# Kernel tuning notes

Hardware: AMD Instinct MI355X
Metric: run time of the kernel (lower is better)

Reference implementation:

```python
import jax, jax.numpy as jnp
import numpy as np

NUM_WIRES = 20
DEPTH = 4


def setup_inputs() -> dict:
    key = jax.random.key(0)
    x = jax.random.normal(key, (NUM_WIRES,), dtype=jnp.float32)
    return {"x": x}


def _apply_1q(state, gate, wire):
    # state: flat [2^n] complex; apply 2x2 gate on `wire`
    s = state.reshape(2 ** wire, 2, -1)
    return jnp.einsum('ab,ibj->iaj', gate, s).reshape(-1)


def _apply_cnot(state, control):
    # CNOT on adjacent wires (control, control+1): flip target where control==1
    s = state.reshape(2 ** control, 2, 2, -1)
    s = jnp.concatenate([s[:, :1], s[:, 1:, ::-1]], axis=1)
    return s.reshape(-1)


def _simulate(x):
    n = NUM_WIRES
    state = jnp.zeros(2 ** n, dtype=jnp.complex64).at[0].set(1.0)
    half = (x.astype(jnp.float32) * 0.5)
    c = jnp.cos(half).astype(jnp.complex64)  # [n]
    s = jnp.sin(half).astype(jnp.complex64)  # [n]
    for _ in range(DEPTH):
        for w in range(n):
            cw, sw = c[w], s[w]
            rx = jnp.stack([jnp.stack([cw, -1j * sw]), jnp.stack([-1j * sw, cw])])
            ry = jnp.stack([jnp.stack([cw, -sw]), jnp.stack([sw, cw])])
            state = _apply_1q(state, rx, w)
            state = _apply_1q(state, ry, w)
        for w in range(n - 1):
            state = _apply_cnot(state, w)
    probs = jnp.abs(state) ** 2  # real float32 [2^n]
    expz = []
    for i in range(n):
        p = probs.reshape(2 ** i, 2, -1).sum(axis=(0, 2))
        expz.append(p[0] - p[1])
    return jnp.stack(expz).astype(jnp.float32)  # [n] <Z_i>


def reference(x):
    return _simulate(x)
```

## Files before the change

kernel.cpp:

```cpp
#include <hip/hip_runtime.h>


#define NW 20

__device__ __forceinline__ float2 cmul(float2 a, float2 b) {
    return make_float2(a.x*b.x - a.y*b.y, a.x*b.y + a.y*b.x);
}

__device__ __forceinline__ void apply_gate(float2& a0, float2& a1,
                                           float2 u00, float2 u01,
                                           float2 u10, float2 u11) {
    float2 b0, b1;
    b0.x = u00.x*a0.x - u00.y*a0.y + u01.x*a1.x - u01.y*a1.y;
    b0.y = u00.x*a0.y + u00.y*a0.x + u01.x*a1.y + u01.y*a1.x;
    b1.x = u10.x*a0.x - u10.y*a0.y + u11.x*a1.x - u11.y*a1.y;
    b1.y = u10.x*a0.y + u10.y*a0.x + u11.x*a1.y + u11.y*a1.x;
    a0 = b0; a1 = b1;
}

__device__ __forceinline__ float2 shflx(float2 v, int m) {
    float2 r;
    r.x = __shfl_xor(v.x, m, 64);
    r.y = __shfl_xor(v.y, m, 64);
    return r;
}

__device__ __forceinline__ unsigned sfx(unsigned x) {
    x ^= x >> 1; x ^= x >> 2; x ^= x >> 4; x ^= x >> 8; x ^= x >> 16; return x;
}

template<int A>
__device__ __forceinline__ void gate_regbit4(float2 (&amp)[4], const float2* Gw) {
    float2 u00 = Gw[0], u01 = Gw[1], u10 = Gw[2], u11 = Gw[3];
    #pragma unroll
    for (int r = 0; r < 4; r++)
        if (!(r & (1 << A)))
            apply_gate(amp[r], amp[r | (1 << A)], u00, u01, u10, u11);
}

template<int A, int LM>
__device__ __forceinline__ void swap_reg_lane4(float2 (&amp)[4], unsigned lane) {
    bool hb = (lane & (unsigned)LM) != 0u;
    #pragma unroll
    for (int r = 0; r < 4; r++) {
        if (!(r & (1 << A))) {
            float2 lo = amp[r], hi = amp[r | (1 << A)];
            float2 xs = hb ? lo : hi;
            float2 ys = shflx(xs, LM);
            amp[r]            = hb ? ys : lo;
            amp[r | (1 << A)] = hb ? hi : ys;
        }
    }
}

__device__ __forceinline__ void prep_Gs(const float* __restrict__ x, float2* Gs,
                                        unsigned t) {
    if (t < NW) {
        float h = 0.5f * x[t];
        float c = cosf(h), s = sinf(h);
        float cc = c*c, ss = s*s, cs = c*s;
        Gs[t*4+0] = make_float2(cc,  ss);
        Gs[t*4+1] = make_float2(-cs, -cs);
        Gs[t*4+2] = make_float2(cs,  -cs);
        Gs[t*4+3] = make_float2(cc,  -ss);
    }
}

template<int MODE>
__global__ __launch_bounds__(1024) void stageA(const float* __restrict__ x,
                                               const float2* __restrict__ src,
                                               float2* __restrict__ dst) {
    __shared__ float2 lds[4096];
    __shared__ float2 Gs[4*NW];
    const unsigned t = threadIdx.x;
    prep_Gs(x, Gs, t);
    __syncthreads();
    const unsigned lane = t & 63u, wv = t >> 6;
    const unsigned w0 = wv & 1u, w1 = (wv >> 1) & 1u, w2 = (wv >> 2) & 1u, w3 = wv >> 3;
    const unsigned H   = blockIdx.x;
    const unsigned Hp  = H ^ (H >> 1);
    const unsigned inj = (H & 1u) << 11;
    const unsigned lb  = (wv << 8) | (lane << 2);
    const unsigned gb  = (lb ^ (lb >> 1)) ^ inj;

    float2 amp[4];
    if (MODE == 1) {
        const float4* q = (const float4*)(src + ((size_t)Hp << 12) + (gb & ~3u));
        float4 q0 = q[0], q1 = q[1];
        float2 e0 = make_float2(q0.x,q0.y), e1 = make_float2(q0.z,q0.w);
        float2 e2 = make_float2(q1.x,q1.y), e3 = make_float2(q1.z,q1.w);
        bool s2 = (gb & 2u) != 0u;
        amp[0] = s2 ? e2 : e0;
        amp[1] = s2 ? e3 : e1;
        amp[2] = s2 ? e1 : e3;
        amp[3] = s2 ? e0 : e2;
    } else {
        float2 P = make_float2(1.0f, 0.0f);
        #pragma unroll
        for (int b = 12; b <= 19; b++)
            P = cmul(P, Gs[(19-b)*4 + (int)((Hp >> (b-12)) & 1u)*2]);
        #pragma unroll
        for (int b = 2; b <= 11; b++)
            P = cmul(P, Gs[(19-b)*4 + (int)((gb >> b) & 1u)*2]);
        float2 T[4];
        #pragma unroll
        for (int j = 0; j < 4; j++)
            T[j] = cmul(P, cmul(Gs[19*4 + (j&1)*2], Gs[18*4 + ((j>>1)&1)*2]));
        bool s2 = (gb & 2u) != 0u;
        amp[0] = s2 ? T[2] : T[0];
        amp[1] = s2 ? T[3] : T[1];
        amp[2] = s2 ? T[1] : T[3];
        amp[3] = s2 ? T[0] : T[2];
    }

    gate_regbit4<0>(amp, Gs + 19*4);
    gate_regbit4<1>(amp, Gs + 18*4);
    swap_reg_lane4<0,1>(amp, lane);
    swap_reg_lane4<1,2>(amp, lane);
    gate_regbit4<0>(amp, Gs + 17*4);
    gate_regbit4<1>(amp, Gs + 16*4);
    swap_reg_lane4<0,4>(amp, lane);
    swap_reg_lane4<1,8>(amp, lane);
    gate_regbit4<0>(amp, Gs + 15*4);
    gate_regbit4<1>(amp, Gs + 14*4);
    swap_reg_lane4<0,16>(amp, lane);
    swap_reg_lane4<1,32>(amp, lane);
    gate_regbit4<0>(amp, Gs + 13*4);
    gate_regbit4<1>(amp, Gs + 12*4);
    #pragma unroll
    for (int k = 0; k < 4; k++) lds[lane | ((unsigned)k << 6) | (wv << 8)] = amp[k];
    __syncthreads();
    #pragma unroll
    for (int k = 0; k < 4; k++)
        amp[k] = lds[lane | (w0 << 6) | (w1 << 7) | ((unsigned)k << 8) | (w2 << 10) | (w3 << 11)];
    gate_regbit4<0>(amp, Gs + 11*4);
    gate_regbit4<1>(amp, Gs + 10*4);
    __syncthreads();
    #pragma unroll
    for (int k = 0; k < 4; k++) lds[lane | ((unsigned)k << 6) | (wv << 8)] = amp[k];
    __syncthreads();
    #pragma unroll
    for (int k = 0; k < 4; k++)
        amp[k] = lds[lane | (w2 << 6) | (w3 << 7) | (w0 << 8) | (w1 << 9) | ((unsigned)k << 10)];
    gate_regbit4<0>(amp, Gs + 9*4);
    gate_regbit4<1>(amp, Gs + 8*4);
    float2* d = dst + ((size_t)H << 12);
    #pragma unroll
    for (int k = 0; k < 4; k++)
        d[lane | (w0 << 6) | (w1 << 7) | (w2 << 8) | (w3 << 9) | ((unsigned)k << 10)] = amp[k];
}

template<int FUSE>
__global__ __launch_bounds__(1024) void stageB(const float* __restrict__ x,
                                               float2* __restrict__ st,
                                               float* __restrict__ partial) {
    __shared__ float2 lds[4096];
    __shared__ float2 Gs[4*NW];
    const unsigned t = threadIdx.x;
    prep_Gs(x, Gs, t);
    __syncthreads();
    const unsigned lane = t & 63u, wv = t >> 6;
    const unsigned w0 = wv & 1u, w1 = (wv >> 1) & 1u, w2 = (wv >> 2) & 1u, w3 = wv >> 3;
    const unsigned bb = blockIdx.x;
    const unsigned m = lane & 15u, l4 = (lane >> 4) & 1u, l5 = lane >> 5;

    float2 amp[4];
    #pragma unroll
    for (int k = 0; k < 4; k++) {
        unsigned h = (unsigned)k | (l4 << 2) | (l5 << 3) | (wv << 4);
        amp[k] = st[((size_t)h << 12) | (bb << 4) | m];
    }
    gate_regbit4<0>(amp, Gs + 7*4);
    gate_regbit4<1>(amp, Gs + 6*4);
    swap_reg_lane4<0,16>(amp, lane);
    swap_reg_lane4<1,32>(amp, lane);
    gate_regbit4<0>(amp, Gs + 5*4);
    gate_regbit4<1>(amp, Gs + 4*4);
    #pragma unroll
    for (int k = 0; k < 4; k++) lds[lane | ((unsigned)k << 6) | (wv << 8)] = amp[k];
    __syncthreads();
    #pragma unroll
    for (int k = 0; k < 4; k++)
        amp[k] = lds[lane | (w0 << 6) | (w1 << 7) | ((unsigned)k << 8) | (w2 << 10) | (w3 << 11)];
    gate_regbit4<0>(amp, Gs + 3*4);
    gate_regbit4<1>(amp, Gs + 2*4);
    __syncthreads();
    #pragma unroll
    for (int k = 0; k < 4; k++) lds[lane | ((unsigned)k << 6) | (wv << 8)] = amp[k];
    __syncthreads();
    #pragma unroll
    for (int k = 0; k < 4; k++)
        amp[k] = lds[lane | (w2 << 6) | (w3 << 7) | (w0 << 8) | (w1 << 9) | ((unsigned)k << 10)];
    gate_regbit4<0>(amp, Gs + 1*4);
    gate_regbit4<1>(amp, Gs + 0*4);

    if (!FUSE) {
        #pragma unroll
        for (int k = 0; k < 4; k++) {
            unsigned h = l4 | (l5 << 1) | (w0 << 2) | (w1 << 3) | (w2 << 4) | (w3 << 5)
                       | (((unsigned)k & 1u) << 6) | (((unsigned)k >> 1) << 7);
            st[((size_t)h << 12) | (bb << 4) | m] = amp[k];
        }
    } else {
        float p[4];
        #pragma unroll
        for (int k = 0; k < 4; k++) p[k] = amp[k].x*amp[k].x + amp[k].y*amp[k].y;
        float S19 = (p[0] + p[1]) - (p[2] + p[3]);
        float D   = p[0] - p[1] - p[2] + p[3];
        unsigned v = m | (bb << 4) | (l4 << 12) | (l5 << 13) | (w0 << 14)
                   | (w1 << 15) | (w2 << 16) | (w3 << 17);
        unsigned cm = sfx(v);
        float acc[NW];
        acc[0] = S19; acc[1] = D;
        #pragma unroll
        for (int w = 2; w < NW; w++)
            acc[w] = ((cm >> (19 - w)) & 1u) ? -D : D;

        __syncthreads();
        float* red = (float*)lds;
        #pragma unroll
        for (int w = 0; w < NW; w++) {
            float s = acc[w];
            #pragma unroll
            for (int off = 32; off; off >>= 1) s += __shfl_down(s, off, 64);
            if (lane == 0) red[wv*NW + w] = s;
        }
        __syncthreads();
        if (t < NW) {
            float s = 0.0f;
            #pragma unroll
            for (int v16 = 0; v16 < 16; v16++) s += red[v16*NW + (int)t];
            partial[bb*NW + t] = s;
        }
    }
}

__global__ __launch_bounds__(256) void reduce_out(const float* __restrict__ partial,
                                                  float* __restrict__ out) {
    __shared__ float red[4*NW];
    unsigned t = threadIdx.x;
    float vals[NW];
    #pragma unroll
    for (int w = 0; w < NW; w++) vals[w] = partial[t*NW + w];
    #pragma unroll
    for (int w = 0; w < NW; w++) {
        float v = vals[w];
        #pragma unroll
        for (int off = 32; off; off >>= 1) v += __shfl_down(v, off, 64);
        if ((t & 63u) == 0u) red[(t >> 6)*NW + w] = v;
    }
    __syncthreads();
    if (t < NW) out[t] = red[t] + red[NW+t] + red[2*NW+t] + red[3*NW+t];
}

extern "C" void kernel_launch(void* const* d_in, const int* in_sizes, int n_in,
                              void* d_out, int out_size, void* d_ws, size_t ws_size,
                              hipStream_t stream) {
    (void)in_sizes; (void)n_in; (void)out_size; (void)ws_size;
    const float* x = (const float*)d_in[0];
    float* out = (float*)d_out;

    char* ws = (char*)d_ws;
    float*  partial = (float*)(ws + 1024);
    float2* buf0    = (float2*)(ws + 65536);
    float2* buf1    = (float2*)(ws + 65536 + (size_t)(8u << 20));

    stageA<0><<<256, 1024, 0, stream>>>(x, buf1 , buf0);
    stageB<0><<<256, 1024, 0, stream>>>(x, buf0, nullptr);
    stageA<1><<<256, 1024, 0, stream>>>(x, buf0, buf1);
    stageB<0><<<256, 1024, 0, stream>>>(x, buf1, nullptr);
    stageA<1><<<256, 1024, 0, stream>>>(x, buf1, buf0);
    stageB<1><<<256, 1024, 0, stream>>>(x, buf0, partial);
    reduce_out<<<1, 256, 0, stream>>>(partial, out);
}
```

Measured before the change: 63.68 us.

## Fuse final reduction via atomic ticket, vectorize complex gates, hoist loads before sync

```diff
diff --git a/kernel.cpp b/kernel.cpp
--- a/kernel.cpp
+++ b/kernel.cpp
@@ -3,23 +3,14 @@
 
 #define NW 20
 
-__device__ __forceinline__ float2 cmul(float2 a, float2 b) {
-    return make_float2(a.x*b.x - a.y*b.y, a.x*b.y + a.y*b.x);
-}
-
-__device__ __forceinline__ void apply_gate(float2& a0, float2& a1,
-                                           float2 u00, float2 u01,
-                                           float2 u10, float2 u11) {
-    float2 b0, b1;
-    b0.x = u00.x*a0.x - u00.y*a0.y + u01.x*a1.x - u01.y*a1.y;
-    b0.y = u00.x*a0.y + u00.y*a0.x + u01.x*a1.y + u01.y*a1.x;
-    b1.x = u10.x*a0.x - u10.y*a0.y + u11.x*a1.x - u11.y*a1.y;
-    b1.y = u10.x*a0.y + u10.y*a0.x + u11.x*a1.y + u11.y*a1.x;
-    a0 = b0; a1 = b1;
-}
-
-__device__ __forceinline__ float2 shflx(float2 v, int m) {
-    float2 r;
+typedef float f2v __attribute__((ext_vector_type(2)));
+
+__device__ __forceinline__ f2v csw(f2v a) { return __builtin_shufflevector(a, a, 1, 0); }
+
+__device__ __forceinline__ f2v pcm(f2v a, f2v ru, f2v iu) { return ru*a + iu*csw(a); }
+
+__device__ __forceinline__ f2v shflx2(f2v v, int m) {
+    f2v r;
     r.x = __shfl_xor(v.x, m, 64);
     r.y = __shfl_xor(v.y, m, 64);
     return r;
@@ -30,51 +21,53 @@
 }
 
 template<int A>
-__device__ __forceinline__ void gate_regbit4(float2 (&amp)[4], const float2* Gw) {
-    float2 u00 = Gw[0], u01 = Gw[1], u10 = Gw[2], u11 = Gw[3];
+__device__ __forceinline__ void gate4(f2v (&amp)[4], const f2v* g) {
+    f2v r00=g[0], i00=g[1], r01=g[2], i01=g[3], r10=g[4], i10=g[5], r11=g[6], i11=g[7];
     #pragma unroll
     for (int r = 0; r < 4; r++)
-        if (!(r & (1 << A)))
-            apply_gate(amp[r], amp[r | (1 << A)], u00, u01, u10, u11);
+        if (!(r & (1 << A))) {
+            f2v a0 = amp[r], a1 = amp[r | (1 << A)];
+            f2v a0s = csw(a0), a1s = csw(a1);
+            amp[r]            = r00*a0 + i00*a0s + r01*a1 + i01*a1s;
+            amp[r | (1 << A)] = r10*a0 + i10*a0s + r11*a1 + i11*a1s;
+        }
 }
 
 template<int A, int LM>
-__device__ __forceinline__ void swap_reg_lane4(float2 (&amp)[4], unsigned lane) {
+__device__ __forceinline__ void swap_reg_lane4(f2v (&amp)[4], unsigned lane) {
     bool hb = (lane & (unsigned)LM) != 0u;
     #pragma unroll
     for (int r = 0; r < 4; r++) {
         if (!(r & (1 << A))) {
-            float2 lo = amp[r], hi = amp[r | (1 << A)];
-            float2 xs = hb ? lo : hi;
-            float2 ys = shflx(xs, LM);
+            f2v lo = amp[r], hi = amp[r | (1 << A)];
+            f2v xs = hb ? lo : hi;
+            f2v ys = shflx2(xs, LM);
             amp[r]            = hb ? ys : lo;
             amp[r | (1 << A)] = hb ? hi : ys;
         }
     }
 }
 
-__device__ __forceinline__ void prep_Gs(const float* __restrict__ x, float2* Gs,
-                                        unsigned t) {
+__device__ __forceinline__ void prep_Gp(const float* __restrict__ x, f2v* Gp, unsigned t) {
     if (t < NW) {
         float h = 0.5f * x[t];
         float c = cosf(h), s = sinf(h);
         float cc = c*c, ss = s*s, cs = c*s;
-        Gs[t*4+0] = make_float2(cc,  ss);
-        Gs[t*4+1] = make_float2(-cs, -cs);
-        Gs[t*4+2] = make_float2(cs,  -cs);
-        Gs[t*4+3] = make_float2(cc,  -ss);
+        Gp[t*8+0] = f2v{cc, cc};    Gp[t*8+1] = f2v{-ss, ss};
+        Gp[t*8+2] = f2v{-cs, -cs};  Gp[t*8+3] = f2v{cs, -cs};
+        Gp[t*8+4] = f2v{cs, cs};    Gp[t*8+5] = f2v{cs, -cs};
+        Gp[t*8+6] = f2v{cc, cc};    Gp[t*8+7] = f2v{ss, -ss};
     }
 }
 
 template<int MODE>
 __global__ __launch_bounds__(1024) void stageA(const float* __restrict__ x,
                                                const float2* __restrict__ src,
-                                               float2* __restrict__ dst) {
-    __shared__ float2 lds[4096];
-    __shared__ float2 Gs[4*NW];
+                                               float2* __restrict__ dst,
+                                               unsigned* __restrict__ ticket) {
+    __shared__ f2v lds[4096];
+    __shared__ f2v Gp[8*NW];
     const unsigned t = threadIdx.x;
-    prep_Gs(x, Gs, t);
-    __syncthreads();
     const unsigned lane = t & 63u, wv = t >> 6;
     const unsigned w0 = wv & 1u, w1 = (wv >> 1) & 1u, w2 = (wv >> 2) & 1u, w3 = wv >> 3;
     const unsigned H   = blockIdx.x;
@@ -83,29 +76,43 @@
     const unsigned lb  = (wv << 8) | (lane << 2);
     const unsigned gb  = (lb ^ (lb >> 1)) ^ inj;
 
-    float2 amp[4];
+    if (MODE == 0 && H == 0 && t == 0) *ticket = 0u;
+
+    float4 q0, q1;
     if (MODE == 1) {
         const float4* q = (const float4*)(src + ((size_t)Hp << 12) + (gb & ~3u));
-        float4 q0 = q[0], q1 = q[1];
-        float2 e0 = make_float2(q0.x,q0.y), e1 = make_float2(q0.z,q0.w);
-        float2 e2 = make_float2(q1.x,q1.y), e3 = make_float2(q1.z,q1.w);
+        q0 = q[0]; q1 = q[1];
+    }
+    prep_Gp(x, Gp, t);
+    __syncthreads();
+
+    f2v amp[4];
+    if (MODE == 1) {
+        f2v e0 = f2v{q0.x,q0.y}, e1 = f2v{q0.z,q0.w};
+        f2v e2 = f2v{q1.x,q1.y}, e3 = f2v{q1.z,q1.w};
         bool s2 = (gb & 2u) != 0u;
         amp[0] = s2 ? e2 : e0;
         amp[1] = s2 ? e3 : e1;
         amp[2] = s2 ? e1 : e3;
         amp[3] = s2 ? e0 : e2;
     } else {
-        float2 P = make_float2(1.0f, 0.0f);
-        #pragma unroll
-        for (int b = 12; b <= 19; b++)
-            P = cmul(P, Gs[(19-b)*4 + (int)((Hp >> (b-12)) & 1u)*2]);
-        #pragma unroll
-        for (int b = 2; b <= 11; b++)
-            P = cmul(P, Gs[(19-b)*4 + (int)((gb >> b) & 1u)*2]);
-        float2 T[4];
-        #pragma unroll
-        for (int j = 0; j < 4; j++)
-            T[j] = cmul(P, cmul(Gs[19*4 + (j&1)*2], Gs[18*4 + ((j>>1)&1)*2]));
+        f2v P = f2v{1.0f, 0.0f};
+        #pragma unroll
+        for (int b = 12; b <= 19; b++) {
+            int w = 19 - b, bit = (int)((Hp >> (b-12)) & 1u);
+            P = pcm(P, Gp[w*8 + bit*4], Gp[w*8 + bit*4 + 1]);
+        }
+        #pragma unroll
+        for (int b = 2; b <= 11; b++) {
+            int w = 19 - b, bit = (int)((gb >> b) & 1u);
+            P = pcm(P, Gp[w*8 + bit*4], Gp[w*8 + bit*4 + 1]);
+        }
+        f2v T[4];
+        #pragma unroll
+        for (int j = 0; j < 4; j++) {
+            f2v v = pcm(P, Gp[19*8 + (j&1)*4], Gp[19*8 + (j&1)*4 + 1]);
+            T[j]  = pcm(v, Gp[18*8 + ((j>>1)&1)*4], Gp[18*8 + ((j>>1)&1)*4 + 1]);
+        }
         bool s2 = (gb & 2u) != 0u;
         amp[0] = s2 ? T[2] : T[0];
         amp[1] = s2 ? T[3] : T[1];
@@ -113,28 +120,28 @@
         amp[3] = s2 ? T[0] : T[2];
     }
 
-    gate_regbit4<0>(amp, Gs + 19*4);
-    gate_regbit4<1>(amp, Gs + 18*4);
+    gate4<0>(amp, Gp + 19*8);
+    gate4<1>(amp, Gp + 18*8);
     swap_reg_lane4<0,1>(amp, lane);
     swap_reg_lane4<1,2>(amp, lane);
-    gate_regbit4<0>(amp, Gs + 17*4);
-    gate_regbit4<1>(amp, Gs + 16*4);
+    gate4<0>(amp, Gp + 17*8);
+    gate4<1>(amp, Gp + 16*8);
     swap_reg_lane4<0,4>(amp, lane);
     swap_reg_lane4<1,8>(amp, lane);
-    gate_regbit4<0>(amp, Gs + 15*4);
-    gate_regbit4<1>(amp, Gs + 14*4);
+    gate4<0>(amp, Gp + 15*8);
+    gate4<1>(amp, Gp + 14*8);
     swap_reg_lane4<0,16>(amp, lane);
     swap_reg_lane4<1,32>(amp, lane);
-    gate_regbit4<0>(amp, Gs + 13*4);
-    gate_regbit4<1>(amp, Gs + 12*4);
+    gate4<0>(amp, Gp + 13*8);
+    gate4<1>(amp, Gp + 12*8);
     #pragma unroll
     for (int k = 0; k < 4; k++) lds[lane | ((unsigned)k << 6) | (wv << 8)] = amp[k];
     __syncthreads();
     #pragma unroll
     for (int k = 0; k < 4; k++)
         amp[k] = lds[lane | (w0 << 6) | (w1 << 7) | ((unsigned)k << 8) | (w2 << 10) | (w3 << 11)];
-    gate_regbit4<0>(amp, Gs + 11*4);
-    gate_regbit4<1>(amp, Gs + 10*4);
+    gate4<0>(amp, Gp + 11*8);
+    gate4<1>(amp, Gp + 10*8);
     __syncthreads();
     #pragma unroll
     for (int k = 0; k < 4; k++) lds[lane | ((unsigned)k << 6) | (wv << 8)] = amp[k];
@@ -142,9 +149,9 @@
     #pragma unroll
     for (int k = 0; k < 4; k++)
         amp[k] = lds[lane | (w2 << 6) | (w3 << 7) | (w0 << 8) | (w1 << 9) | ((unsigned)k << 10)];
-    gate_regbit4<0>(amp, Gs + 9*4);
-    gate_regbit4<1>(amp, Gs + 8*4);
-    float2* d = dst + ((size_t)H << 12);
+    gate4<0>(amp, Gp + 9*8);
+    gate4<1>(amp, Gp + 8*8);
+    f2v* d = (f2v*)dst + ((size_t)H << 12);
     #pragma unroll
     for (int k = 0; k < 4; k++)
         d[lane | (w0 << 6) | (w1 << 7) | (w2 << 8) | (w3 << 9) | ((unsigned)k << 10)] = amp[k];
@@ -153,37 +160,42 @@
 template<int FUSE>
 __global__ __launch_bounds__(1024) void stageB(const float* __restrict__ x,
                                                float2* __restrict__ st,
-                                               float* __restrict__ partial) {
-    __shared__ float2 lds[4096];
-    __shared__ float2 Gs[4*NW];
+                                               float* __restrict__ partial,
+                                               float* __restrict__ out,
+                                               unsigned* __restrict__ ticket) {
+    __shared__ f2v lds[4096];
+    __shared__ f2v Gp[8*NW];
+    __shared__ unsigned islast;
     const unsigned t = threadIdx.x;
-    prep_Gs(x, Gs, t);
-    __syncthreads();
     const unsigned lane = t & 63u, wv = t >> 6;
     const unsigned w0 = wv & 1u, w1 = (wv >> 1) & 1u, w2 = (wv >> 2) & 1u, w3 = wv >> 3;
     const unsigned bb = blockIdx.x;
     const unsigned m = lane & 15u, l4 = (lane >> 4) & 1u, l5 = lane >> 5;
 
-    float2 amp[4];
+    f2v amp[4];
+    f2v* stv = (f2v*)st;
     #pragma unroll
     for (int k = 0; k < 4; k++) {
         unsigned h = (unsigned)k | (l4 << 2) | (l5 << 3) | (wv << 4);
-        amp[k] = st[((size_t)h << 12) | (bb << 4) | m];
-    }
-    gate_regbit4<0>(amp, Gs + 7*4);
-    gate_regbit4<1>(amp, Gs + 6*4);
+        amp[k] = stv[((size_t)h << 12) | (bb << 4) | m];
+    }
+    prep_Gp(x, Gp, t);
+    __syncthreads();
+
+    gate4<0>(amp, Gp + 7*8);
+    gate4<1>(amp, Gp + 6*8);
     swap_reg_lane4<0,16>(amp, lane);
     swap_reg_lane4<1,32>(amp, lane);
-    gate_regbit4<0>(amp, Gs + 5*4);
-    gate_regbit4<1>(amp, Gs + 4*4);
+    gate4<0>(amp, Gp + 5*8);
+    gate4<1>(amp, Gp + 4*8);
     #pragma unroll
     for (int k = 0; k < 4; k++) lds[lane | ((unsigned)k << 6) | (wv << 8)] = amp[k];
     __syncthreads();
     #pragma unroll
     for (int k = 0; k < 4; k++)
         amp[k] = lds[lane | (w0 << 6) | (w1 << 7) | ((unsigned)k << 8) | (w2 << 10) | (w3 << 11)];
-    gate_regbit4<0>(amp, Gs + 3*4);
-    gate_regbit4<1>(amp, Gs + 2*4);
+    gate4<0>(amp, Gp + 3*8);
+    gate4<1>(amp, Gp + 2*8);
     __syncthreads();
     #pragma unroll
     for (int k = 0; k < 4; k++) lds[lane | ((unsigned)k << 6) | (wv << 8)] = amp[k];
@@ -191,15 +203,15 @@
     #pragma unroll
     for (int k = 0; k < 4; k++)
         amp[k] = lds[lane | (w2 << 6) | (w3 << 7) | (w0 << 8) | (w1 << 9) | ((unsigned)k << 10)];
-    gate_regbit4<0>(amp, Gs + 1*4);
-    gate_regbit4<1>(amp, Gs + 0*4);
+    gate4<0>(amp, Gp + 1*8);
+    gate4<1>(amp, Gp + 0*8);
 
     if (!FUSE) {
         #pragma unroll
         for (int k = 0; k < 4; k++) {
             unsigned h = l4 | (l5 << 1) | (w0 << 2) | (w1 << 3) | (w2 << 4) | (w3 << 5)
                        | (((unsigned)k & 1u) << 6) | (((unsigned)k >> 1) << 7);
-            st[((size_t)h << 12) | (bb << 4) | m] = amp[k];
+            stv[((size_t)h << 12) | (bb << 4) | m] = amp[k];
         }
     } else {
         float p[4];
@@ -232,25 +244,31 @@
             for (int v16 = 0; v16 < 16; v16++) s += red[v16*NW + (int)t];
             partial[bb*NW + t] = s;
         }
-    }
-}
-
-__global__ __launch_bounds__(256) void reduce_out(const float* __restrict__ partial,
-                                                  float* __restrict__ out) {
-    __shared__ float red[4*NW];
-    unsigned t = threadIdx.x;
-    float vals[NW];
-    #pragma unroll
-    for (int w = 0; w < NW; w++) vals[w] = partial[t*NW + w];
-    #pragma unroll
-    for (int w = 0; w < NW; w++) {
-        float v = vals[w];
-        #pragma unroll
-        for (int off = 32; off; off >>= 1) v += __shfl_down(v, off, 64);
-        if ((t & 63u) == 0u) red[(t >> 6)*NW + w] = v;
-    }
-    __syncthreads();
-    if (t < NW) out[t] = red[t] + red[NW+t] + red[2*NW+t] + red[3*NW+t];
+        __threadfence();
+        __syncthreads();
+        if (t == 0) islast = (atomicAdd(ticket, 1u) == 255u) ? 1u : 0u;
+        __syncthreads();
+        if (islast) {
+            float vals[NW];
+            #pragma unroll
+            for (int w = 0; w < NW; w++)
+                vals[w] = (t < 256u) ? partial[t*NW + w] : 0.0f;
+            #pragma unroll
+            for (int w = 0; w < NW; w++) {
+                float s = vals[w];
+                #pragma unroll
+                for (int off = 32; off; off >>= 1) s += __shfl_down(s, off, 64);
+                if (lane == 0) red[wv*NW + w] = s;
+            }
+            __syncthreads();
+            if (t < NW) {
+                float s = 0.0f;
+                #pragma unroll
+                for (int v16 = 0; v16 < 16; v16++) s += red[v16*NW + (int)t];
+                out[t] = s;
+            }
+        }
+    }
 }
 
 extern "C" void kernel_launch(void* const* d_in, const int* in_sizes, int n_in,
@@ -261,15 +279,15 @@
     float* out = (float*)d_out;
 
     char* ws = (char*)d_ws;
-    float*  partial = (float*)(ws + 1024);
-    float2* buf0    = (float2*)(ws + 65536);
-    float2* buf1    = (float2*)(ws + 65536 + (size_t)(8u << 20));
-
-    stageA<0><<<256, 1024, 0, stream>>>(x, buf1 , buf0);
-    stageB<0><<<256, 1024, 0, stream>>>(x, buf0, nullptr);
-    stageA<1><<<256, 1024, 0, stream>>>(x, buf0, buf1);
-    stageB<0><<<256, 1024, 0, stream>>>(x, buf1, nullptr);
-    stageA<1><<<256, 1024, 0, stream>>>(x, buf1, buf0);
-    stageB<1><<<256, 1024, 0, stream>>>(x, buf0, partial);
-    reduce_out<<<1, 256, 0, stream>>>(partial, out);
-}
+    unsigned* ticket = (unsigned*)(ws + 512);
+    float*  partial  = (float*)(ws + 1024);
+    float2* buf0     = (float2*)(ws + 65536);
+    float2* buf1     = (float2*)(ws + 65536 + (size_t)(8u << 20));
+
+    stageA<0><<<256, 1024, 0, stream>>>(x, buf1 , buf0, ticket);
+    stageB<0><<<256, 1024, 0, stream>>>(x, buf0, nullptr, nullptr, nullptr);
+    stageA<1><<<256, 1024, 0, stream>>>(x, buf0, buf1, nullptr);
+    stageB<0><<<256, 1024, 0, stream>>>(x, buf1, nullptr, nullptr, nullptr);
+    stageA<1><<<256, 1024, 0, stream>>>(x, buf1, buf0, nullptr);
+    stageB<1><<<256, 1024, 0, stream>>>(x, buf0, partial, out, ticket);
+}
```

Result: slower. 125.8 us (+97.6%).
